# Performance work log

Measured on AMD Instinct MI355X. Metric: run time of the kernel, lower is better.

Reference implementation:

```python
import jax, jax.numpy as jnp
import numpy as np

B, D, NCOMP, DCOMP = 4096, 2048, 4, 1024  # out_features = NCOMP * DCOMP = 4096


def setup_inputs() -> dict:
    key = jax.random.key(0)
    ks = jax.random.split(key, 6)
    scale = 0.02
    return {
        "x": jax.random.normal(ks[0], (B, D), jnp.float32),
        "noise": jax.random.normal(ks[1], (B, NCOMP), jnp.float32),
        "Wc": jax.random.normal(ks[2], (NCOMP, D, DCOMP), jnp.float32) * scale,
        "bc": jnp.zeros((NCOMP, DCOMP), jnp.float32),
        "Wg": jax.random.normal(ks[3], (D, NCOMP), jnp.float32) * scale,
        "bg": jnp.zeros((NCOMP,), jnp.float32),
        "Wn": jax.random.normal(ks[4], (D, NCOMP), jnp.float32) * scale,
        "bn": jnp.zeros((NCOMP,), jnp.float32),
    }


def reference(x, noise, Wc, bc, Wg, bg, Wn, bn):
    # gating: H = Wg(x) + randn * softplus(Wnoise(x))
    g = x @ Wg + bg                                   # [B, n]
    sp = jax.nn.softplus(x @ Wn + bn)                 # [B, n]
    H = g + noise * sp                                # [B, n]
    # top-1 index, monotonic hard gate: select all components i <= argmax
    k = jnp.argmax(H, axis=1, keepdims=True)          # [B, 1]
    mask = (jnp.arange(H.shape[1])[None, :] <= k).astype(H.dtype)  # [B, n]
    # straight-through: forward value = mask, grad d G/d H = identity
    G = H + jax.lax.stop_gradient(mask - H)
    # all components computed vectorized; unselected ones are zeroed by G
    comps = jnp.einsum('bd,ndo->bno', x, Wc) + bc     # [B, n, DCOMP]
    mask_sg = jax.lax.stop_gradient(mask)
    # multiply by mask_sg so unselected (padded) channels carry no grad path,
    # matching torch which never computes components beyond k (zero pad).
    E = (comps * G[:, :, None] * mask_sg[:, :, None]).reshape(x.shape[0], -1)  # [B, out_features]
    return (E, G)
```

## Files before the change

kernel.cpp:

```cpp
#include <hip/hip_runtime.h>
#include <hip/hip_bf16.h>
#include <math.h>

constexpr int BROWS = 4096;
constexpr int DDIM  = 2048;
constexpr int NCOMP = 4;
constexpr int DCOMP = 1024;
constexpr int NOUT  = NCOMP * DCOMP;

typedef __attribute__((ext_vector_type(8))) short bf16x8;
typedef __attribute__((ext_vector_type(4))) float f32x4;
typedef __attribute__((ext_vector_type(4))) short s16x4;

__device__ __forceinline__ short f2bf(float f) {
  union { float f; unsigned u; } v; v.f = f;
  unsigned r = v.u + 0x7FFFu + ((v.u >> 16) & 1u);
  return (short)(r >> 16);
}

#define GLOAD_LDS16(gptr, lptr) __builtin_amdgcn_global_load_lds( \
    (const __attribute__((address_space(1))) void*)(gptr),        \
    (__attribute__((address_space(3))) void*)(lptr), 16, 0, 0)

__global__ __launch_bounds__(256) void prep_kernel(
    const float* __restrict__ x, const float* __restrict__ noise,
    const float* __restrict__ Wg, const float* __restrict__ bg,
    const float* __restrict__ Wn, const float* __restrict__ bn,
    const float* __restrict__ Wc,
    float* __restrict__ Gout, short* __restrict__ xb, short* __restrict__ WcT) {
  __shared__ float tile[64][65];
  const int bid = blockIdx.x;
  const int tid = threadIdx.x;

  if (bid < 1024) {
    const int lane = tid & 63;
    const int row  = bid * 4 + (tid >> 6);
    const float* xr = x + (size_t)row * DDIM;
    short* xbr = xb + (size_t)row * DDIM;

    float ag[4] = {0.f, 0.f, 0.f, 0.f};
    float an[4] = {0.f, 0.f, 0.f, 0.f};
#pragma unroll
    for (int i = 0; i < 8; i++) {
      int d = i * 256 + lane * 4;
      float4 v = *reinterpret_cast<const float4*>(xr + d);
      s16x4 s; s.x = f2bf(v.x); s.y = f2bf(v.y); s.z = f2bf(v.z); s.w = f2bf(v.w);
      *reinterpret_cast<s16x4*>(xbr + d) = s;
      float xv[4] = {v.x, v.y, v.z, v.w};
#pragma unroll
      for (int j = 0; j < 4; j++) {
        float4 wg = *reinterpret_cast<const float4*>(Wg + 4 * (d + j));
        float4 wn = *reinterpret_cast<const float4*>(Wn + 4 * (d + j));
        ag[0] += xv[j] * wg.x; ag[1] += xv[j] * wg.y;
        ag[2] += xv[j] * wg.z; ag[3] += xv[j] * wg.w;
        an[0] += xv[j] * wn.x; an[1] += xv[j] * wn.y;
        an[2] += xv[j] * wn.z; an[3] += xv[j] * wn.w;
      }
    }
#pragma unroll
    for (int off = 32; off > 0; off >>= 1) {
#pragma unroll
      for (int c = 0; c < 4; c++) {
        ag[c] += __shfl_xor(ag[c], off);
        an[c] += __shfl_xor(an[c], off);
      }
    }
    if (lane == 0) {
      float H[4];
#pragma unroll
      for (int c = 0; c < 4; c++) {
        float v  = an[c] + bn[c];
        float sp = (v > 20.f) ? v : log1pf(expf(v));
        H[c] = (ag[c] + bg[c]) + noise[(size_t)row * NCOMP + c] * sp;
      }
      int k = 0; float best = H[0];
#pragma unroll
      for (int c = 1; c < 4; c++) { if (H[c] > best) { best = H[c]; k = c; } }
#pragma unroll
      for (int c = 0; c < 4; c++)
        Gout[(size_t)row * NCOMP + c] = (c <= k) ? 1.0f : 0.0f;
    }
  } else {
    const int tb  = bid - 1024;
    const int o_t = tb & 15, d_t = (tb >> 4) & 31, c = tb >> 9;
    const int d0 = d_t * 64, o0 = o_t * 64;
    const int col = tid & 63, rb = tid >> 6;

    const float* src = Wc + ((size_t)c * DDIM + d0) * DCOMP + o0;
#pragma unroll
    for (int i = 0; i < 16; i++) {
      int r = rb + i * 4;
      tile[r][col] = src[(size_t)r * DCOMP + col];
    }
    __syncthreads();
    short* dst = WcT + ((size_t)c * DCOMP + o0) * DDIM + d0;
    const int o  = tid >> 2;
    const int dsb = (tid & 3) * 16;
    bf16x8 p0, p1;
#pragma unroll
    for (int k = 0; k < 8; k++) {
      p0[k] = f2bf(tile[dsb + k][o]);
      p1[k] = f2bf(tile[dsb + 8 + k][o]);
    }
    *reinterpret_cast<bf16x8*>(dst + (size_t)o * DDIM + dsb)     = p0;
    *reinterpret_cast<bf16x8*>(dst + (size_t)o * DDIM + dsb + 8) = p1;
  }
}

constexpr int BM = 256, BN = 256, BK = 64;
constexpr int NT = DDIM / BK;
constexpr int HS = 128 * 64;

template<int MB, int NB>
__device__ __forceinline__ void MF(f32x4 (&acc)[8][4], bf16x8 (&a)[4][2], bf16x8 (&b)[2][2]) {
#pragma unroll
  for (int kh = 0; kh < 2; kh++)
#pragma unroll
    for (int ml = 0; ml < 4; ml++)
#pragma unroll
      for (int nl = 0; nl < 2; nl++)
        acc[MB + ml][NB + nl] = __builtin_amdgcn_mfma_f32_16x16x32_bf16(
            a[ml][kh], b[nl][kh], acc[MB + ml][NB + nl], 0, 0, 0);
}

#define PH_SYNC_MFMA(MB, NB)                                 \
  __builtin_amdgcn_s_barrier();                              \
  asm volatile("s_waitcnt lgkmcnt(0)" ::: "memory");         \
  __builtin_amdgcn_sched_barrier(0);                         \
  __builtin_amdgcn_s_setprio(1);                             \
  MF<MB, NB>(acc, a, b);                                     \
  __builtin_amdgcn_s_setprio(0);                             \
  __builtin_amdgcn_sched_barrier(0);

__global__ __launch_bounds__(512, 2) void gemm_kernel(
    const short* __restrict__ xb, const short* __restrict__ wt,
    const float* __restrict__ bc, const float* __restrict__ G,
    float* __restrict__ E) {
  __shared__ short Asm[2][2][HS];
  __shared__ short Bsm[2][2][HS];

  const int tid  = threadIdx.x;
  const int wave = tid >> 6, lane = tid & 63;
  const int wm = wave >> 2, wn = wave & 3;
  const int fr = lane & 15, fq = lane >> 4, l7 = lane & 7;

  const int swz = (blockIdx.x & 7) * 32 + (blockIdx.x >> 3);
  const int trow0 = (swz >> 4) * BM;
  const int tcol0 = (swz & 15) * BN;

  const short* baseA[2] = { xb + (size_t)(trow0      ) * DDIM,
                            xb + (size_t)(trow0 + 128) * DDIM };
  const short* baseB[2] = { wt + (size_t)(tcol0      ) * DDIM,
                            wt + (size_t)(tcol0 + 128) * DDIM };

  size_t soff[2]; int ldst[2];
#pragma unroll
  for (int l = 0; l < 2; l++) {
    int f = l * 512 + tid;
    int r = f >> 3;
    int s = (f & 7) ^ (r & 7);
    soff[l] = (size_t)r * DDIM + s * 8;
    ldst[l] = (l * 512 + wave * 64) * 8;
  }

  auto STAGE = [&](const short* gb, int t, short* ldsh) {
#pragma unroll
    for (int l = 0; l < 2; l++)
      GLOAD_LDS16(gb + t * 64 + soff[l], ldsh + ldst[l]);
  };
  auto LDA = [&](const short* Ah, bf16x8 (&a)[4][2]) {
#pragma unroll
    for (int ml = 0; ml < 4; ml++) {
      int rh = wm * 64 + ml * 16 + fr;
#pragma unroll
      for (int kh = 0; kh < 2; kh++) {
        int sl = ((kh * 4 + fq) ^ l7) * 8;
        a[ml][kh] = *reinterpret_cast<const bf16x8*>(Ah + rh * 64 + sl);
      }
    }
  };
  auto LDB = [&](const short* Bh, bf16x8 (&b)[2][2]) {
#pragma unroll
    for (int nl = 0; nl < 2; nl++) {
      int ch = wn * 32 + nl * 16 + fr;
#pragma unroll
      for (int kh = 0; kh < 2; kh++) {
        int sl = ((kh * 4 + fq) ^ l7) * 8;
        b[nl][kh] = *reinterpret_cast<const bf16x8*>(Bh + ch * 64 + sl);
      }
    }
  };

  f32x4 acc[8][4];
#pragma unroll
  for (int m = 0; m < 8; m++)
#pragma unroll
    for (int n = 0; n < 4; n++) acc[m][n] = f32x4{0.f, 0.f, 0.f, 0.f};
  bf16x8 a[4][2], b[2][2];

  STAGE(baseA[0], 0, &Asm[0][0][0]);
  STAGE(baseA[1], 0, &Asm[0][1][0]);
  STAGE(baseB[0], 0, &Bsm[0][0][0]);
  STAGE(baseB[1], 0, &Bsm[0][1][0]);
  STAGE(baseA[0], 1, &Asm[1][0][0]);
  STAGE(baseB[1], 1, &Bsm[1][1][0]);
  asm volatile("s_waitcnt vmcnt(4)" ::: "memory");
  __builtin_amdgcn_s_barrier();

  for (int i = 0; i < NT / 2; i++) {
    const int t1 = 2 * i + 1, t2 = 2 * i + 2, t3 = 2 * i + 3;
    const bool more = (i < NT / 2 - 1);

    LDA(&Asm[0][0][0], a); LDB(&Bsm[0][0][0], b);
    STAGE(baseA[1], t1, &Asm[1][1][0]);
    PH_SYNC_MFMA(0, 0);
    __builtin_amdgcn_s_barrier();
    LDB(&Bsm[0][1][0], b);
    STAGE(baseB[0], t1, &Bsm[1][0][0]);
    PH_SYNC_MFMA(0, 2);
    __builtin_amdgcn_s_barrier();
    LDA(&Asm[0][1][0], a);
    if (more) STAGE(baseA[0], t2, &Asm[0][0][0]);
    PH_SYNC_MFMA(4, 2);
    __builtin_amdgcn_s_barrier();
    LDB(&Bsm[0][0][0], b);
    if (more) STAGE(baseB[1], t2, &Bsm[0][1][0]);
    PH_SYNC_MFMA(4, 0);
    if (more) { asm volatile("s_waitcnt vmcnt(4)" ::: "memory"); }
    else      { asm volatile("s_waitcnt vmcnt(0)" ::: "memory"); }
    __builtin_amdgcn_s_barrier();
    LDA(&Asm[1][0][0], a); LDB(&Bsm[1][0][0], b);
    if (more) STAGE(baseA[1], t2, &Asm[0][1][0]);
    PH_SYNC_MFMA(0, 0);
    __builtin_amdgcn_s_barrier();
    LDB(&Bsm[1][1][0], b);
    if (more) STAGE(baseB[0], t2, &Bsm[0][0][0]);
    PH_SYNC_MFMA(0, 2);
    __builtin_amdgcn_s_barrier();
    LDA(&Asm[1][1][0], a);
    if (more) STAGE(baseA[0], t3, &Asm[1][0][0]);
    PH_SYNC_MFMA(4, 2);
    __builtin_amdgcn_s_barrier();
    LDB(&Bsm[1][0][0], b);
    if (more) STAGE(baseB[1], t3, &Bsm[1][1][0]);
    PH_SYNC_MFMA(4, 0);
    if (more) { asm volatile("s_waitcnt vmcnt(4)" ::: "memory"); }
    __builtin_amdgcn_s_barrier();
  }

  const int comp = tcol0 >> 10;
  const float* __restrict__ bcn = bc + (size_t)comp * DCOMP + (tcol0 & (DCOMP - 1));
  float bias[4];
#pragma unroll
  for (int n = 0; n < 4; n++)
    bias[n] = bcn[((n >> 1) * 128) + wn * 32 + (n & 1) * 16 + fr];
#pragma unroll
  for (int m = 0; m < 8; m++) {
    int growb = trow0 + ((m >> 2) * 128) + wm * 64 + (m & 3) * 16 + fq * 4;
#pragma unroll
    for (int j = 0; j < 4; j++) {
      int r = growb + j;
      float mval = G[(size_t)r * NCOMP + comp];
      float* Erow = E + (size_t)r * NOUT + tcol0;
#pragma unroll
      for (int n = 0; n < 4; n++) {
        int coll = ((n >> 1) * 128) + wn * 32 + (n & 1) * 16 + fr;
        Erow[coll] = mval * (acc[m][n][j] + bias[n]);
      }
    }
  }
}

extern "C" void kernel_launch(void* const* d_in, const int* in_sizes, int n_in,
                              void* d_out, int out_size, void* d_ws, size_t ws_size,
                              hipStream_t stream) {
  const float* x     = (const float*)d_in[0];
  const float* noise = (const float*)d_in[1];
  const float* Wc    = (const float*)d_in[2];
  const float* bc    = (const float*)d_in[3];
  const float* Wg    = (const float*)d_in[4];
  const float* bg    = (const float*)d_in[5];
  const float* Wn    = (const float*)d_in[6];
  const float* bn    = (const float*)d_in[7];

  float* E = (float*)d_out;
  float* G = (float*)d_out + (size_t)BROWS * NOUT;

  short* xb  = (short*)d_ws;
  short* WcT = xb + (size_t)BROWS * DDIM;

  prep_kernel<<<3072, 256, 0, stream>>>(x, noise, Wg, bg, Wn, bn, Wc, G, xb, WcT);
  gemm_kernel<<<256, 512, 0, stream>>>(xb, WcT, bc, G, E);
}
```

Measured before the change: 97.66 us.

## Peel last K iteration, relax MFMA scheduling fences, and remap tiles per XCD

```diff
diff --git a/kernel.cpp b/kernel.cpp
--- a/kernel.cpp
+++ b/kernel.cpp
@@ -125,12 +125,10 @@
 
 #define PH_SYNC_MFMA(MB, NB)                                 \
   __builtin_amdgcn_s_barrier();                              \
-  asm volatile("s_waitcnt lgkmcnt(0)" ::: "memory");         \
-  __builtin_amdgcn_sched_barrier(0);                         \
+  asm volatile("s_waitcnt lgkmcnt(0)");                      \
   __builtin_amdgcn_s_setprio(1);                             \
   MF<MB, NB>(acc, a, b);                                     \
-  __builtin_amdgcn_s_setprio(0);                             \
-  __builtin_amdgcn_sched_barrier(0);
+  __builtin_amdgcn_s_setprio(0);
 
 __global__ __launch_bounds__(512, 2) void gemm_kernel(
     const short* __restrict__ xb, const short* __restrict__ wt,
@@ -144,9 +142,9 @@
   const int wm = wave >> 2, wn = wave & 3;
   const int fr = lane & 15, fq = lane >> 4, l7 = lane & 7;
 
-  const int swz = (blockIdx.x & 7) * 32 + (blockIdx.x >> 3);
-  const int trow0 = (swz >> 4) * BM;
-  const int tcol0 = (swz & 15) * BN;
+  const int xcd = blockIdx.x & 7, j = blockIdx.x >> 3;
+  const int trow0 = (((xcd >> 1) << 2) + (j & 3)) * BM;
+  const int tcol0 = (((xcd & 1) << 3) + (j >> 2)) * BN;
 
   const short* baseA[2] = { xb + (size_t)(trow0      ) * DDIM,
                             xb + (size_t)(trow0 + 128) * DDIM };
@@ -207,9 +205,8 @@
   asm volatile("s_waitcnt vmcnt(4)" ::: "memory");
   __builtin_amdgcn_s_barrier();
 
-  for (int i = 0; i < NT / 2; i++) {
+  for (int i = 0; i < NT / 2 - 1; i++) {
     const int t1 = 2 * i + 1, t2 = 2 * i + 2, t3 = 2 * i + 3;
-    const bool more = (i < NT / 2 - 1);
 
     LDA(&Asm[0][0][0], a); LDB(&Bsm[0][0][0], b);
     STAGE(baseA[1], t1, &Asm[1][1][0]);
@@ -220,32 +217,60 @@
     PH_SYNC_MFMA(0, 2);
     __builtin_amdgcn_s_barrier();
     LDA(&Asm[0][1][0], a);
-    if (more) STAGE(baseA[0], t2, &Asm[0][0][0]);
+    STAGE(baseA[0], t2, &Asm[0][0][0]);
     PH_SYNC_MFMA(4, 2);
     __builtin_amdgcn_s_barrier();
     LDB(&Bsm[0][0][0], b);
-    if (more) STAGE(baseB[1], t2, &Bsm[0][1][0]);
+    STAGE(baseB[1], t2, &Bsm[0][1][0]);
     PH_SYNC_MFMA(4, 0);
-    if (more) { asm volatile("s_waitcnt vmcnt(4)" ::: "memory"); }
-    else      { asm volatile("s_waitcnt vmcnt(0)" ::: "memory"); }
+    asm volatile("s_waitcnt vmcnt(4)" ::: "memory");
     __builtin_amdgcn_s_barrier();
     LDA(&Asm[1][0][0], a); LDB(&Bsm[1][0][0], b);
-    if (more) STAGE(baseA[1], t2, &Asm[0][1][0]);
+    STAGE(baseA[1], t2, &Asm[0][1][0]);
     PH_SYNC_MFMA(0, 0);
     __builtin_amdgcn_s_barrier();
     LDB(&Bsm[1][1][0], b);
-    if (more) STAGE(baseB[0], t2, &Bsm[0][0][0]);
+    STAGE(baseB[0], t2, &Bsm[0][0][0]);
     PH_SYNC_MFMA(0, 2);
     __builtin_amdgcn_s_barrier();
     LDA(&Asm[1][1][0], a);
-    if (more) STAGE(baseA[0], t3, &Asm[1][0][0]);
+    STAGE(baseA[0], t3, &Asm[1][0][0]);
     PH_SYNC_MFMA(4, 2);
     __builtin_amdgcn_s_barrier();
     LDB(&Bsm[1][0][0], b);
-    if (more) STAGE(baseB[1], t3, &Bsm[1][1][0]);
+    STAGE(baseB[1], t3, &Bsm[1][1][0]);
     PH_SYNC_MFMA(4, 0);
-    if (more) { asm volatile("s_waitcnt vmcnt(4)" ::: "memory"); }
-    __builtin_amdgcn_s_barrier();
+    asm volatile("s_waitcnt vmcnt(4)" ::: "memory");
+    __builtin_amdgcn_s_barrier();
+  }
+
+  {
+    LDA(&Asm[0][0][0], a); LDB(&Bsm[0][0][0], b);
+    STAGE(baseA[1], NT - 1, &Asm[1][1][0]);
+    PH_SYNC_MFMA(0, 0);
+    __builtin_amdgcn_s_barrier();
+    LDB(&Bsm[0][1][0], b);
+    STAGE(baseB[0], NT - 1, &Bsm[1][0][0]);
+    PH_SYNC_MFMA(0, 2);
+    __builtin_amdgcn_s_barrier();
+    LDA(&Asm[0][1][0], a);
+    PH_SYNC_MFMA(4, 2);
+    __builtin_amdgcn_s_barrier();
+    LDB(&Bsm[0][0][0], b);
+    PH_SYNC_MFMA(4, 0);
+    asm volatile("s_waitcnt vmcnt(0)" ::: "memory");
+    __builtin_amdgcn_s_barrier();
+    LDA(&Asm[1][0][0], a); LDB(&Bsm[1][0][0], b);
+    PH_SYNC_MFMA(0, 0);
+    __builtin_amdgcn_s_barrier();
+    LDB(&Bsm[1][1][0], b);
+    PH_SYNC_MFMA(0, 2);
+    __builtin_amdgcn_s_barrier();
+    LDA(&Asm[1][1][0], a);
+    PH_SYNC_MFMA(4, 2);
+    __builtin_amdgcn_s_barrier();
+    LDB(&Bsm[1][0][0], b);
+    PH_SYNC_MFMA(4, 0);
   }
 
   const int comp = tcol0 >> 10;
```

Result: faster. 95.62 us (-2.1%).
